# Kernel tuning notes

Hardware: AMD Instinct MI355X
Metric: run time of the kernel (lower is better)

## Reference

```python
import jax, jax.numpy as jnp
import numpy as np

B, T, C = 8, 2048, 1024
HEAD = 64
BLOCK = 2048  # block_size == max_size == ramp_size


def setup_inputs() -> dict:
    key = jax.random.key(0)
    kx, kq, kk, kv = jax.random.split(key, 4)
    x = jax.random.normal(kx, (B, T, C), dtype=jnp.float32)
    # torch Linear(n_embd, head_size, bias=False): store as (C, HEAD) for x @ W
    s = 1.0 / np.sqrt(C)
    Wq = jax.random.uniform(kq, (C, HEAD), dtype=jnp.float32, minval=-s, maxval=s)
    Wk = jax.random.uniform(kk, (C, HEAD), dtype=jnp.float32, minval=-s, maxval=s)
    Wv = jax.random.uniform(kv, (C, HEAD), dtype=jnp.float32, minval=-s, maxval=s)
    # adaptive_span current_val parameter, shape (1,1,1), init 0
    current_val = jnp.zeros((1, 1, 1), dtype=jnp.float32)
    return {"x": x, "Wq": Wq, "Wk": Wk, "Wv": Wv, "current_val": current_val}


def reference(x, Wq, Wk, Wv, current_val):
    Bb, Tt, Cc = x.shape
    q = x @ Wq  # (B,T,H)
    k = x @ Wk
    v = x @ Wv
    scale = 1.0 / jnp.sqrt(jnp.asarray(HEAD, dtype=x.dtype))
    scores = jnp.einsum('bth,bsh->bts', q, k) * scale  # (B,T,T)
    causal = jnp.tril(jnp.ones((Tt, Tt), dtype=bool))
    scores = jnp.where(causal, scores, -jnp.inf)
    w = jax.nn.softmax(scores, axis=-1)
    # adaptive span post-softmax mask (T == max_size here, so no slicing)
    template = jnp.linspace(1.0 - BLOCK, 0.0, BLOCK, dtype=x.dtype)  # (T,)
    span = template + current_val * BLOCK  # (1,1,T)
    span = jnp.clip(span / BLOCK + 1.0, 0.0, 1.0)
    w = w * span
    w = w / (w.sum(-1, keepdims=True) + 1e-8)
    # dropout p=0 (eval) -> identity
    out = jnp.einsum('bts,bsh->bth', w, v)  # (B,T,H)
    return out
```

## Files before the change

### kernel.cpp

```cpp
#include <hip/hip_runtime.h>
#include <hip/hip_bf16.h>

#define BSZ 8
#define T 2048
#define C 1024
#define H 64
#define M (BSZ*T)

typedef __attribute__((ext_vector_type(4))) float f32x4;
typedef __attribute__((ext_vector_type(8))) short bf16x8;
typedef __attribute__((ext_vector_type(4))) short s16x4;
typedef __attribute__((ext_vector_type(8))) short s16x8;

static __device__ __forceinline__ short f2bf(float f) {
  union { float f; unsigned u; } c; c.f = f;
  unsigned u = c.u;
  u = (u + 0x7fffu + ((u >> 16) & 1u)) >> 16;
  return (short)u;
}

__global__ __launch_bounds__(256) void k_wt(const float* __restrict__ Wq,
                                            const float* __restrict__ Wk,
                                            const float* __restrict__ Wv,
                                            short* __restrict__ wt) {
  int idx = blockIdx.x * 256 + threadIdx.x;
  int c = idx & (C - 1);
  int n = idx >> 10;
  int w = n >> 6;
  int h = n & (H - 1);
  const float* W = (w == 0) ? Wq : (w == 1) ? Wk : Wv;
  wt[idx] = f2bf(W[c * H + h]);
}

__global__ __launch_bounds__(256) void k_qkv(const float* __restrict__ x,
                                             const short* __restrict__ wt,
                                             short* __restrict__ qb,
                                             short* __restrict__ kb,
                                             short* __restrict__ vt) {
  __shared__ short xs[2][32 * 64];
  __shared__ short wl[2][192 * 64];
  const int tid = threadIdx.x;
  const int m0 = blockIdx.x * 32;
  const int lane = tid & 63;
  const int wid = tid >> 6;
  const int g16 = lane >> 4, l16 = lane & 15;
  const int row0 = (wid & 1) * 16;
  const int nc0 = (wid >> 1) * 96;

  f32x4 acc[6];
  #pragma unroll
  for (int i = 0; i < 6; ++i) acc[i] = (f32x4){0.f, 0.f, 0.f, 0.f};

  const int xr = tid >> 4;
  const int xc4 = (tid & 15) * 4;
  const int xsw = xc4 ^ ((xr & 7) << 3);
  const int wr = tid >> 3;
  const int wc8 = (tid & 7) * 8;
  const int wsw = wc8 ^ ((wr & 7) << 3);
  const int fsw = (l16 & 7) << 3;

  float4 xA0, xA1, xB0, xB1;
  s16x8 wA0, wA1, wA2, wA3, wA4, wA5;
  s16x8 wB0, wB1, wB2, wB3, wB4, wB5;

#define QKV_LOAD(S, kc) do { \
    x##S##0 = *(const float4*)&x[(size_t)(m0 + xr) * C + (kc) + xc4]; \
    x##S##1 = *(const float4*)&x[(size_t)(m0 + xr + 16) * C + (kc) + xc4]; \
    w##S##0 = *(const s16x8*)&wt[(wr +   0) * C + (kc) + wc8]; \
    w##S##1 = *(const s16x8*)&wt[(wr +  32) * C + (kc) + wc8]; \
    w##S##2 = *(const s16x8*)&wt[(wr +  64) * C + (kc) + wc8]; \
    w##S##3 = *(const s16x8*)&wt[(wr +  96) * C + (kc) + wc8]; \
    w##S##4 = *(const s16x8*)&wt[(wr + 128) * C + (kc) + wc8]; \
    w##S##5 = *(const s16x8*)&wt[(wr + 160) * C + (kc) + wc8]; \
  } while (0)

#define QKV_STORE(S, buf) do { \
    s16x4 h0 = { f2bf((x##S##0).x), f2bf((x##S##0).y), f2bf((x##S##0).z), f2bf((x##S##0).w) }; \
    s16x4 h1 = { f2bf((x##S##1).x), f2bf((x##S##1).y), f2bf((x##S##1).z), f2bf((x##S##1).w) }; \
    *(s16x4*)&xs[buf][xr * 64 + xsw] = h0; \
    *(s16x4*)&xs[buf][(xr + 16) * 64 + xsw] = h1; \
    *(s16x8*)&wl[buf][(wr +   0) * 64 + wsw] = w##S##0; \
    *(s16x8*)&wl[buf][(wr +  32) * 64 + wsw] = w##S##1; \
    *(s16x8*)&wl[buf][(wr +  64) * 64 + wsw] = w##S##2; \
    *(s16x8*)&wl[buf][(wr +  96) * 64 + wsw] = w##S##3; \
    *(s16x8*)&wl[buf][(wr + 128) * 64 + wsw] = w##S##4; \
    *(s16x8*)&wl[buf][(wr + 160) * 64 + wsw] = w##S##5; \
  } while (0)

#define QKV_COMPUTE(buf) do { \
    _Pragma("unroll") \
    for (int ks = 0; ks < 2; ++ks) { \
      bf16x8 a = *(const bf16x8*)&xs[buf][(row0 + l16) * 64 + ((ks * 32 + g16 * 8) ^ fsw)]; \
      _Pragma("unroll") \
      for (int nt = 0; nt < 6; ++nt) { \
        bf16x8 bfr = *(const bf16x8*)&wl[buf][(nc0 + nt * 16 + l16) * 64 + ((ks * 32 + g16 * 8) ^ fsw)]; \
        acc[nt] = __builtin_amdgcn_mfma_f32_16x16x32_bf16(a, bfr, acc[nt], 0, 0, 0); \
      } \
    } \
  } while (0)

  QKV_LOAD(A, 0);
  QKV_STORE(A, 0);
  QKV_LOAD(B, 64);
  __syncthreads();

  #pragma unroll 1
  for (int ii = 0; ii < 8; ++ii) {
    if (ii < 7) QKV_LOAD(A, (2 * ii + 2) * 64);
    QKV_STORE(B, 1);
    QKV_COMPUTE(0);
    __syncthreads();
    if (ii < 7) {
      QKV_LOAD(B, (2 * ii + 3) * 64);
      QKV_STORE(A, 0);
    }
    QKV_COMPUTE(1);
    if (ii < 7) __syncthreads();
  }
#undef QKV_LOAD
#undef QKV_STORE
#undef QKV_COMPUTE

  const int r0 = row0 + g16 * 4;
  #pragma unroll
  for (int nt = 0; nt < 6; ++nt) {
    const int nglob = nc0 + nt * 16;
    const int which = nglob >> 6;
    const int col = (nglob & 63) + l16;
    #pragma unroll
    for (int j = 0; j < 4; ++j) {
      const int tg = m0 + r0 + j;
      const short val = f2bf(acc[nt][j]);
      if (which == 0)      qb[tg * H + col] = val;
      else if (which == 1) kb[tg * H + col] = val;
      else {
        const int b = tg >> 11, tl = tg & (T - 1);
        vt[((b << 6) + col) * T + tl] = val;
      }
    }
  }
}

__global__ __launch_bounds__(512, 4) void k_attn(const short* __restrict__ qb,
                                                 const short* __restrict__ kb,
                                                 const short* __restrict__ vt,
                                                 const float* __restrict__ cvp,
                                                 float* __restrict__ out) {
  __shared__ short plds[8][2][16][40];
  __shared__ float mw[8][16];
  __shared__ float Lw[8][16];
  __shared__ float Ow[8][16][68];
  const int blk = blockIdx.x;
  const int b = blk & 7;
  const int t = 127 - (blk >> 3);
  const int q0 = t << 4;
  const int tid = threadIdx.x;
  const int wid = tid >> 6;
  const int lane = tid & 63;
  const int g16 = lane >> 4, l16 = lane & 15;
  const float cv = cvp[0];
  const float SCL = 0.125f * 1.44269504f;

  const int nit = (q0 + 16 + 31) >> 5;
  const int npw = (nit + 7) >> 3;
  const int lo = wid * npw;
  const int hi = (lo + npw < nit) ? lo + npw : nit;

  const short* qp = qb + ((size_t)(b << 11) + q0 + l16) * H + g16 * 8;
  bf16x8 qf0 = *(const bf16x8*)qp;
  bf16x8 qf1 = *(const bf16x8*)(qp + 32);
  const int qg = q0 + l16;

  float m = -3e38f, L = 0.f;
  f32x4 O[4];
  #pragma unroll
  for (int t4 = 0; t4 < 4; ++t4) O[t4] = (f32x4){0.f, 0.f, 0.f, 0.f};

  if (lo < hi) {
    const short* kp = kb + ((size_t)(b << 11) + lo * 32 + l16) * H + g16 * 8;
    const short* vp = vt + ((size_t)(b << 6) + l16) * T + lo * 32 + g16 * 8;
    bf16x8 kc0 = *(const bf16x8*)kp;
    bf16x8 kc1 = *(const bf16x8*)(kp + 32);
    bf16x8 kc2 = *(const bf16x8*)(kp + 16 * H);
    bf16x8 kc3 = *(const bf16x8*)(kp + 16 * H + 32);
    kp += 32 * H;

    for (int it = lo; it < hi; ++it) {
      bf16x8 kn0, kn1, kn2, kn3;
      const bool more = (it + 1 < hi);
      if (more) {
        kn0 = *(const bf16x8*)kp;
        kn1 = *(const bf16x8*)(kp + 32);
        kn2 = *(const bf16x8*)(kp + 16 * H);
        kn3 = *(const bf16x8*)(kp + 16 * H + 32);
      }
      bf16x8 v0 = *(const bf16x8*)vp;
      bf16x8 v1 = *(const bf16x8*)(vp + 16 * T);
      bf16x8 v2 = *(const bf16x8*)(vp + 32 * T);
      bf16x8 v3 = *(const bf16x8*)(vp + 48 * T);

      f32x4 s0 = {0.f,0.f,0.f,0.f}, s1 = {0.f,0.f,0.f,0.f};
      s0 = __builtin_amdgcn_mfma_f32_16x16x32_bf16(kc0, qf0, s0, 0, 0, 0);
      s0 = __builtin_amdgcn_mfma_f32_16x16x32_bf16(kc1, qf1, s0, 0, 0, 0);
      s1 = __builtin_amdgcn_mfma_f32_16x16x32_bf16(kc2, qf0, s1, 0, 0, 0);
      s1 = __builtin_amdgcn_mfma_f32_16x16x32_bf16(kc3, qf1, s1, 0, 0, 0);

      const int kv0 = it << 5;
      const int kvb = kv0 + g16 * 4;
      const bool diag = (kv0 + 31 > q0);
      float sv[8];
      if (diag) {
        #pragma unroll
        for (int r = 0; r < 8; ++r) {
          const int kvg = kvb + ((r >> 2) << 4) + (r & 3);
          const float s = ((r < 4) ? s0[r] : s1[r - 4]) * SCL;
          sv[r] = (kvg <= qg) ? s : -1e30f;
        }
      } else {
        #pragma unroll
        for (int r = 0; r < 8; ++r)
          sv[r] = ((r < 4) ? s0[r] : s1[r - 4]) * SCL;
      }

      float pmax = fmaxf(fmaxf(fmaxf(sv[0], sv[1]), fmaxf(sv[2], sv[3])),
                         fmaxf(fmaxf(sv[4], sv[5]), fmaxf(sv[6], sv[7])));
      if (!__all(pmax <= m + 7.f)) {
        float v = pmax;
        v = fmaxf(v, __shfl_xor(v, 16, 64));
        v = fmaxf(v, __shfl_xor(v, 32, 64));
        const float mn = fmaxf(m, v);
        const float al = exp2f(m - mn);
        m = mn;
        L *= al;
        #pragma unroll
        for (int t4 = 0; t4 < 4; ++t4) O[t4] *= al;
      }

      float p[8];
      #pragma unroll
      for (int r = 0; r < 8; ++r) {
        const int kvg = kvb + ((r >> 2) << 4) + (r & 3);
        const float sp = fminf(fmaxf((float)(kvg + 1) * (1.f / 2048.f) + cv, 0.f), 1.f);
        p[r] = exp2f(sv[r] - m) * sp;
      }
      if (diag) {
        #pragma unroll
        for (int r = 0; r < 8; ++r) {
          const int kvg = kvb + ((r >> 2) << 4) + (r & 3);
          p[r] = (kvg <= qg) ? p[r] : 0.f;
        }
      }
      L += ((p[0] + p[1]) + (p[2] + p[3])) + ((p[4] + p[5]) + (p[6] + p[7]));

      short (*pl)[40] = plds[wid][it & 1];
      #pragma unroll
      for (int r = 0; r < 8; r += 2) {
        union { float f; unsigned u; } a0, a1;
        a0.f = p[r]; a1.f = p[r + 1];
        const unsigned pk = (a0.u >> 16) | (a1.u & 0xffff0000u);
        *(unsigned*)&pl[l16][((r >> 2) << 4) + g16 * 4 + (r & 3)] = pk;
      }
      bf16x8 pa = *(const bf16x8*)&pl[l16][g16 * 8];
      O[0] = __builtin_amdgcn_mfma_f32_16x16x32_bf16(v0, pa, O[0], 0, 0, 0);
      O[1] = __builtin_amdgcn_mfma_f32_16x16x32_bf16(v1, pa, O[1], 0, 0, 0);
      O[2] = __builtin_amdgcn_mfma_f32_16x16x32_bf16(v2, pa, O[2], 0, 0, 0);
      O[3] = __builtin_amdgcn_mfma_f32_16x16x32_bf16(v3, pa, O[3], 0, 0, 0);

      if (more) { kc0 = kn0; kc1 = kn1; kc2 = kn2; kc3 = kn3; }
      kp += 32 * H;
      vp += 32;
    }
  }

  float Lr = L;
  Lr += __shfl_xor(Lr, 16, 64);
  Lr += __shfl_xor(Lr, 32, 64);
  if (g16 == 0) { mw[wid][l16] = m; Lw[wid][l16] = Lr; }
  #pragma unroll
  for (int t4 = 0; t4 < 4; ++t4)
    *(f32x4*)&Ow[wid][l16][t4 * 16 + g16 * 4] = O[t4];
  __syncthreads();

  if (tid < 256) {
    const int r = tid >> 4;
    const int c4 = (tid & 15) << 2;
    float Mx = -3e38f;
    #pragma unroll
    for (int w = 0; w < 8; ++w) Mx = fmaxf(Mx, mw[w][r]);
    float f[8], Ls = 0.f;
    #pragma unroll
    for (int w = 0; w < 8; ++w) {
      f[w] = exp2f(mw[w][r] - Mx);
      Ls += Lw[w][r] * f[w];
    }
    f32x4 o = (f32x4){0.f, 0.f, 0.f, 0.f};
    #pragma unroll
    for (int w = 0; w < 8; ++w) {
      f32x4 ow = *(const f32x4*)&Ow[w][r][c4];
      o += ow * f[w];
    }
    o *= 1.f / (Ls + 1e-30f);
    *(f32x4*)&out[(size_t)((b << 11) + q0 + r) * H + c4] = o;
  }
}

extern "C" void kernel_launch(void* const* d_in, const int* in_sizes, int n_in,
                              void* d_out, int out_size, void* d_ws, size_t ws_size,
                              hipStream_t stream) {
  const float* x  = (const float*)d_in[0];
  const float* Wq = (const float*)d_in[1];
  const float* Wk = (const float*)d_in[2];
  const float* Wv = (const float*)d_in[3];
  const float* cv = (const float*)d_in[4];
  float* out = (float*)d_out;

  char* ws = (char*)d_ws;
  short* qb = (short*)(ws);
  short* kb = (short*)(ws + (size_t)M * H * 2);
  short* vt = (short*)(ws + (size_t)2 * M * H * 2);
  short* wt = (short*)(ws + (size_t)3 * M * H * 2);

  hipLaunchKernelGGL(k_wt, dim3(3 * H * C / 256), dim3(256), 0, stream, Wq, Wk, Wv, wt);
  hipLaunchKernelGGL(k_qkv, dim3(M / 32), dim3(256), 0, stream, x, wt, qb, kb, vt);
  hipLaunchKernelGGL(k_attn, dim3(BSZ * T / 16), dim3(512), 0, stream, qb, kb, vt, cv, out);
}
```

Baseline: 65.91 us.

## Cut LDS footprint in QKV and attention kernels to raise occupancy

The QKV GEMM kernel now keeps a single shared-memory buffer for the weight tile instead of two. The pipeline is reordered so each weight tile store sits between barriers, and the kernel gets a min-blocks launch bound. The attention kernel aliases its P-staging buffer with the output-reduction buffer in one shared array and raises its launch bound from 4 to 8 blocks per CU. Both changes aim to fit more waves per CU. The cost is twice as many barriers per iteration in the QKV loop, plus an extra barrier before reusing the aliased attention buffer, and tighter register limits that may cause spills.

Result: slower. 150.4 us (+128.3%).

```diff
diff --git a/kernel.cpp b/kernel.cpp
--- a/kernel.cpp
+++ b/kernel.cpp
@@ -32,13 +32,13 @@
   wt[idx] = f2bf(W[c * H + h]);
 }
 
-__global__ __launch_bounds__(256) void k_qkv(const float* __restrict__ x,
-                                             const short* __restrict__ wt,
-                                             short* __restrict__ qb,
-                                             short* __restrict__ kb,
-                                             short* __restrict__ vt) {
+__global__ __launch_bounds__(256, 4) void k_qkv(const float* __restrict__ x,
+                                                const short* __restrict__ wt,
+                                                short* __restrict__ qb,
+                                                short* __restrict__ kb,
+                                                short* __restrict__ vt) {
   __shared__ short xs[2][32 * 64];
-  __shared__ short wl[2][192 * 64];
+  __shared__ short wl[192 * 64];
   const int tid = threadIdx.x;
   const int m0 = blockIdx.x * 32;
   const int lane = tid & 63;
@@ -74,48 +74,50 @@
     w##S##5 = *(const s16x8*)&wt[(wr + 160) * C + (kc) + wc8]; \
   } while (0)
 
-#define QKV_STORE(S, buf) do { \
+#define QKV_STORE(S, xbuf) do { \
     s16x4 h0 = { f2bf((x##S##0).x), f2bf((x##S##0).y), f2bf((x##S##0).z), f2bf((x##S##0).w) }; \
     s16x4 h1 = { f2bf((x##S##1).x), f2bf((x##S##1).y), f2bf((x##S##1).z), f2bf((x##S##1).w) }; \
-    *(s16x4*)&xs[buf][xr * 64 + xsw] = h0; \
-    *(s16x4*)&xs[buf][(xr + 16) * 64 + xsw] = h1; \
-    *(s16x8*)&wl[buf][(wr +   0) * 64 + wsw] = w##S##0; \
-    *(s16x8*)&wl[buf][(wr +  32) * 64 + wsw] = w##S##1; \
-    *(s16x8*)&wl[buf][(wr +  64) * 64 + wsw] = w##S##2; \
-    *(s16x8*)&wl[buf][(wr +  96) * 64 + wsw] = w##S##3; \
-    *(s16x8*)&wl[buf][(wr + 128) * 64 + wsw] = w##S##4; \
-    *(s16x8*)&wl[buf][(wr + 160) * 64 + wsw] = w##S##5; \
+    *(s16x4*)&xs[xbuf][xr * 64 + xsw] = h0; \
+    *(s16x4*)&xs[xbuf][(xr + 16) * 64 + xsw] = h1; \
+    *(s16x8*)&wl[(wr +   0) * 64 + wsw] = w##S##0; \
+    *(s16x8*)&wl[(wr +  32) * 64 + wsw] = w##S##1; \
+    *(s16x8*)&wl[(wr +  64) * 64 + wsw] = w##S##2; \
+    *(s16x8*)&wl[(wr +  96) * 64 + wsw] = w##S##3; \
+    *(s16x8*)&wl[(wr + 128) * 64 + wsw] = w##S##4; \
+    *(s16x8*)&wl[(wr + 160) * 64 + wsw] = w##S##5; \
   } while (0)
 
-#define QKV_COMPUTE(buf) do { \
+#define QKV_COMPUTE(xbuf) do { \
     _Pragma("unroll") \
     for (int ks = 0; ks < 2; ++ks) { \
-      bf16x8 a = *(const bf16x8*)&xs[buf][(row0 + l16) * 64 + ((ks * 32 + g16 * 8) ^ fsw)]; \
+      bf16x8 a = *(const bf16x8*)&xs[xbuf][(row0 + l16) * 64 + ((ks * 32 + g16 * 8) ^ fsw)]; \
       _Pragma("unroll") \
       for (int nt = 0; nt < 6; ++nt) { \
-        bf16x8 bfr = *(const bf16x8*)&wl[buf][(nc0 + nt * 16 + l16) * 64 + ((ks * 32 + g16 * 8) ^ fsw)]; \
+        bf16x8 bfr = *(const bf16x8*)&wl[(nc0 + nt * 16 + l16) * 64 + ((ks * 32 + g16 * 8) ^ fsw)]; \
         acc[nt] = __builtin_amdgcn_mfma_f32_16x16x32_bf16(a, bfr, acc[nt], 0, 0, 0); \
       } \
     } \
   } while (0)
 
   QKV_LOAD(A, 0);
+  QKV_LOAD(B, 64);
   QKV_STORE(A, 0);
-  QKV_LOAD(B, 64);
   __syncthreads();
 
   #pragma unroll 1
   for (int ii = 0; ii < 8; ++ii) {
-    if (ii < 7) QKV_LOAD(A, (2 * ii + 2) * 64);
-    QKV_STORE(B, 1);
     QKV_COMPUTE(0);
     __syncthreads();
+    QKV_STORE(B, 1);
+    if (ii < 7) QKV_LOAD(A, (2 * ii + 2) * 64);
+    __syncthreads();
+    QKV_COMPUTE(1);
     if (ii < 7) {
+      __syncthreads();
+      QKV_STORE(A, 0);
       QKV_LOAD(B, (2 * ii + 3) * 64);
-      QKV_STORE(A, 0);
-    }
-    QKV_COMPUTE(1);
-    if (ii < 7) __syncthreads();
+      __syncthreads();
+    }
   }
 #undef QKV_LOAD
 #undef QKV_STORE
@@ -141,15 +143,16 @@
   }
 }
 
-__global__ __launch_bounds__(512, 4) void k_attn(const short* __restrict__ qb,
+__global__ __launch_bounds__(512, 8) void k_attn(const short* __restrict__ qb,
                                                  const short* __restrict__ kb,
                                                  const short* __restrict__ vt,
                                                  const float* __restrict__ cvp,
                                                  float* __restrict__ out) {
-  __shared__ short plds[8][2][16][40];
+  __shared__ __align__(16) char smem[34816];
+  short (*plds)[2][16][40] = (short (*)[2][16][40])smem;
+  float (*Ow)[16][68]      = (float (*)[16][68])smem;
   __shared__ float mw[8][16];
   __shared__ float Lw[8][16];
-  __shared__ float Ow[8][16][68];
   const int blk = blockIdx.x;
   const int b = blk & 7;
   const int t = 127 - (blk >> 3);
@@ -272,6 +275,8 @@
     }
   }
 
+  __syncthreads();
+
   float Lr = L;
   Lr += __shfl_xor(Lr, 16, 64);
   Lr += __shfl_xor(Lr, 32, 64);
```
